# Kernel optimization log

Hardware: AMD Instinct MI355X
Metric: run time of the kernel (lower is better)

The kernel has to match this reference:

```python
import jax, jax.numpy as jnp
import numpy as np

NUM_EXPERTS = 8
TOP_K = 2
P_NORM = 1.0  # moe_normalize_expert_weights
HIDDEN = 1024
FFN_HIDDEN = 2048
BATCH, SEQ = 2, 2048


def setup_inputs() -> dict:
    key = jax.random.key(0)
    ks = jax.random.split(key, 5)
    s = 0.02
    return {
        "x": jax.random.normal(ks[0], (BATCH, SEQ, HIDDEN), dtype=jnp.float32),
        "router_w": jax.random.normal(ks[1], (NUM_EXPERTS, HIDDEN), dtype=jnp.float32) * s,
        "w1": jax.random.normal(ks[2], (NUM_EXPERTS, FFN_HIDDEN, HIDDEN), dtype=jnp.float32) * s,
        "v1": jax.random.normal(ks[3], (NUM_EXPERTS, FFN_HIDDEN, HIDDEN), dtype=jnp.float32) * s,
        "w2": jax.random.normal(ks[4], (NUM_EXPERTS, FFN_HIDDEN, HIDDEN), dtype=jnp.float32) * s,
    }


def reference(x, router_w, w1, v1, w2):
    B, S, H = x.shape
    xf = x.reshape(-1, H)  # [T, H]

    # Router: softmax in fp32, top-k, L-p normalize, cast back.
    logits = xf @ router_w.T  # [T, E]
    probs = jax.nn.softmax(logits.astype(jnp.float32), axis=-1)
    top_w, top_e = jax.lax.top_k(probs, TOP_K)  # [T, K]
    norm = jnp.sum(jnp.abs(top_w) ** P_NORM, axis=-1, keepdims=True) ** (1.0 / P_NORM)
    top_w = (top_w / norm).astype(x.dtype)

    # Per-token combine weight for each expert: c[t,e] = sum_k top_w[t,k]*[top_e[t,k]==e]
    c = jnp.sum(jax.nn.one_hot(top_e, NUM_EXPERTS, dtype=x.dtype) * top_w[..., None], axis=1)  # [T, E]

    # Dense per-expert GLU; routing realized by output gating with c (zero for unrouted tokens).
    out = jnp.zeros_like(xf)
    for e in range(NUM_EXPERTS):
        h = jax.nn.silu(xf @ w1[e].T) * (xf @ v1[e].T)  # [T, F]
        out = out + (h @ w2[e]) * c[:, e:e + 1]  # [T, H]
    return out.reshape(B, S, H)
```

## Files before the change

### kernel.cpp

```cpp
#include <hip/hip_runtime.h>
#include <stdint.h>

#define T_TOKENS 4096
#define HID 1024
#define FFN 2048
#define NE 8

typedef __attribute__((ext_vector_type(8))) short bf16x8;
typedef __attribute__((ext_vector_type(4))) float f32x4;

__device__ __forceinline__ unsigned short f2bf(float f) {
  union { float f; uint32_t u; } v; v.f = f;
  uint32_t r = v.u + 0x7FFFu + ((v.u >> 16) & 1u);
  return (unsigned short)(r >> 16);
}

__device__ __forceinline__ uint32_t pack2(float a, float b) {
  return (uint32_t)f2bf(a) | ((uint32_t)f2bf(b) << 16);
}

__device__ __forceinline__ void gload16(const unsigned short* g, unsigned short* l) {
  __builtin_amdgcn_global_load_lds(
      (const __attribute__((address_space(1))) void*)(g),
      (__attribute__((address_space(3))) void*)(l), 16, 0, 0);
}

__device__ __forceinline__ int frag_off(int r, int g) {
  return r * 32 + ((g ^ ((r >> 1) & 3)) << 3);
}

constexpr size_t XBF_OFF  = 0;
constexpr size_t HBUF_OFF = (size_t)T_TOKENS * HID * 2;
constexpr size_t TOKE_OFF = HBUF_OFF + (size_t)T_TOKENS * 2 * FFN * 2;
constexpr size_t TOKW_OFF = TOKE_OFF + (size_t)T_TOKENS * 2 * 4;
constexpr size_t CNT_OFF  = TOKW_OFF + (size_t)T_TOKENS * 2 * 4;
constexpr size_t OFF_OFF  = CNT_OFF + 64;
constexpr size_t LIST_OFF = OFF_OFF + 64;
constexpr size_t META_END = LIST_OFF + (size_t)NE * T_TOKENS * 4;
constexpr size_t W1BF_OFF = META_END;
constexpr size_t V1BF_OFF = W1BF_OFF + (size_t)NE * FFN * HID * 2;
constexpr size_t W2T_OFF  = V1BF_OFF + (size_t)NE * FFN * HID * 2;
constexpr size_t WS_BIG   = W2T_OFF + (size_t)NE * HID * FFN * 2;
constexpr size_t YBUF_OFF = W1BF_OFF;

__global__ __launch_bounds__(256) void cast_w1v1_kernel(const float* __restrict__ w1,
                                                        const float* __restrict__ v1,
                                                        unsigned short* __restrict__ w1b,
                                                        unsigned short* __restrict__ v1b) {
  constexpr size_t HALF = (size_t)NE * FFN * HID / 8 / 256;
  const float* src = (blockIdx.x < HALF) ? w1 : v1;
  unsigned short* dst = (blockIdx.x < HALF) ? w1b : v1b;
  size_t bi = (blockIdx.x < HALF) ? blockIdx.x : blockIdx.x - HALF;
  size_t i = bi * 256 + threadIdx.x;
  const float4* sv = (const float4*)src;
  float4 a = sv[i * 2], b = sv[i * 2 + 1];
  uint4 o;
  o.x = pack2(a.x, a.y); o.y = pack2(a.z, a.w);
  o.z = pack2(b.x, b.y); o.w = pack2(b.z, b.w);
  ((uint4*)dst)[i] = o;
}

__global__ __launch_bounds__(256) void transpose_cast_w2_kernel(const float* __restrict__ w2,
                                                                unsigned short* __restrict__ w2t) {
  int nb = blockIdx.x;
  int kb = blockIdx.y;
  int e  = blockIdx.z;
  __shared__ unsigned short s[64][68];
  int t = threadIdx.x;
  int tr = t >> 4, tc = (t & 15) * 4;
  const float* src = w2 + ((size_t)e * FFN + kb * 64) * HID + nb * 64;
#pragma unroll
  for (int i = 0; i < 4; ++i) {
    int k = tr + i * 16;
    float4 v = *(const float4*)(src + (size_t)k * HID + tc);
    s[k][tc + 0] = f2bf(v.x); s[k][tc + 1] = f2bf(v.y);
    s[k][tc + 2] = f2bf(v.z); s[k][tc + 3] = f2bf(v.w);
  }
  __syncthreads();
  int n = t >> 2, kc = (t & 3) * 16;
  unsigned short* dst = w2t + ((size_t)e * HID + nb * 64 + n) * FFN + kb * 64 + kc;
  unsigned short tmp[16];
#pragma unroll
  for (int i = 0; i < 16; ++i) tmp[i] = s[kc + i][n];
  uint4 o0, o1;
  o0.x = tmp[0] | (tmp[1] << 16);  o0.y = tmp[2] | (tmp[3] << 16);
  o0.z = tmp[4] | (tmp[5] << 16);  o0.w = tmp[6] | (tmp[7] << 16);
  o1.x = tmp[8] | (tmp[9] << 16);  o1.y = tmp[10] | (tmp[11] << 16);
  o1.z = tmp[12] | (tmp[13] << 16); o1.w = tmp[14] | (tmp[15] << 16);
  *(uint4*)dst = o0;
  *(uint4*)(dst + 8) = o1;
}

__global__ __launch_bounds__(256) void router_kernel(const float* __restrict__ x,
                                                     const float* __restrict__ rw,
                                                     int* __restrict__ tok_e,
                                                     float* __restrict__ tok_w,
                                                     unsigned short* __restrict__ xbf) {
  __shared__ float s_rw[NE * HID];
  int tid = threadIdx.x;
  for (int i = tid; i < NE * HID / 4; i += 256)
    ((float4*)s_rw)[i] = ((const float4*)rw)[i];
  __syncthreads();
  int wave = tid >> 6, lane = tid & 63;
  int t = blockIdx.x * 4 + wave;
  const float* xr = x + (size_t)t * HID;
  unsigned short* xbr = xbf + (size_t)t * HID;
  float acc[NE];
#pragma unroll
  for (int e = 0; e < NE; ++e) acc[e] = 0.0f;
  for (int c = 0; c < HID / 64; ++c) {
    int idx = c * 64 + lane;
    float xv = xr[idx];
    xbr[idx] = f2bf(xv);
#pragma unroll
    for (int e = 0; e < NE; ++e) acc[e] += xv * s_rw[e * HID + idx];
  }
#pragma unroll
  for (int e = 0; e < NE; ++e)
    for (int off = 32; off > 0; off >>= 1) acc[e] += __shfl_down(acc[e], off);
  if (lane == 0) {
    float m = acc[0];
#pragma unroll
    for (int e = 1; e < NE; ++e) m = fmaxf(m, acc[e]);
    float p[NE], Z = 0.0f;
#pragma unroll
    for (int e = 0; e < NE; ++e) { p[e] = expf(acc[e] - m); Z += p[e]; }
    int e0 = 0;
#pragma unroll
    for (int e = 1; e < NE; ++e) if (p[e] > p[e0]) e0 = e;
    int e1 = (e0 == 0) ? 1 : 0;
#pragma unroll
    for (int e = 0; e < NE; ++e) if (e != e0 && p[e] > p[e1]) e1 = e;
    float w0 = p[e0] / Z, w1 = p[e1] / Z;
    float nrm = w0 + w1;
    tok_e[t * 2] = e0; tok_e[t * 2 + 1] = e1;
    tok_w[t * 2] = w0 / nrm; tok_w[t * 2 + 1] = w1 / nrm;
  }
}

__global__ __launch_bounds__(256) void scatter_kernel(const int* __restrict__ tok_e,
                                                      int* __restrict__ counts,
                                                      int* __restrict__ lists) {
  int p = blockIdx.x * 256 + threadIdx.x;
  if (p < T_TOKENS * 2) {
    int e = tok_e[p];
    int pos = atomicAdd(&counts[e], 1);
    lists[e * T_TOKENS + pos] = p;
  }
}

__global__ void offsets_kernel(const int* __restrict__ counts, int* __restrict__ offs) {
  if (threadIdx.x == 0 && blockIdx.x == 0) {
    int r = 0;
    for (int e = 0; e < NE; ++e) { offs[e] = r; r += counts[e]; }
  }
}

__global__ __launch_bounds__(256) void combine_kernel(const float* __restrict__ ybuf,
                                                      float* __restrict__ out) {
  int t = blockIdx.x;
  int c = threadIdx.x;
  const float4* y0 = (const float4*)(ybuf + (size_t)(2 * t) * HID);
  const float4* y1 = (const float4*)(ybuf + (size_t)(2 * t + 1) * HID);
  float4 a = y0[c], b = y1[c];
  float4 r; r.x = a.x + b.x; r.y = a.y + b.y; r.z = a.z + b.z; r.w = a.w + b.w;
  ((float4*)(out + (size_t)t * HID))[c] = r;
}


__global__ __launch_bounds__(512) void gemm1b_kernel(
    const unsigned short* __restrict__ xbf,
    const unsigned short* __restrict__ w1b, const unsigned short* __restrict__ v1b,
    const int* __restrict__ counts, const int* __restrict__ offs,
    const int* __restrict__ lists, unsigned short* __restrict__ hbuf) {
  constexpr int BUFSZ = 128 * 32;
  constexpr int NT = HID / 32;
  int nt = blockIdx.x, mt = blockIdx.y, e = blockIdx.z;
  int ne = counts[e];
  if (mt * 128 >= ne) return;
  __shared__ unsigned short s_a[2 * BUFSZ];
  __shared__ unsigned short s_b1[2 * BUFSZ];
  __shared__ unsigned short s_b2[2 * BUFSZ];
  int tid = threadIdx.x;
  int srow = tid >> 2, slot = tid & 3;
  int lchunk = slot ^ ((srow >> 1) & 3);
  const int* lst = lists + e * T_TOKENS + mt * 128;
  int tok = lst[(mt * 128 + srow < ne) ? srow : 0] >> 1;
  const unsigned short* aptr = xbf + (size_t)tok * HID + lchunk * 8;
  size_t brow = ((size_t)e * FFN + nt * 128 + srow) * HID + lchunk * 8;
  const unsigned short* b1p = w1b + brow;
  const unsigned short* b2p = v1b + brow;

  int lane = tid & 63, wv = tid >> 6;
  int wm = (wv >> 2) * 64, wn = (wv & 3) * 32;
  int rl = lane & 15, g = lane >> 4;
  int aoff[4], boff[2];
#pragma unroll
  for (int m = 0; m < 4; ++m) aoff[m] = frag_off(wm + m * 16 + rl, g);
#pragma unroll
  for (int n = 0; n < 2; ++n) boff[n] = frag_off(wn + n * 16 + rl, g);

  f32x4 zero = {0.0f, 0.0f, 0.0f, 0.0f};
  f32x4 acc1[4][2], acc2[4][2];
#pragma unroll
  for (int i = 0; i < 4; ++i)
#pragma unroll
    for (int j = 0; j < 2; ++j) { acc1[i][j] = zero; acc2[i][j] = zero; }

  auto stage = [&](int s, int t) {
    int off = t * 32;
    gload16(aptr + off, s_a  + s * BUFSZ + tid * 8);
    gload16(b1p  + off, s_b1 + s * BUFSZ + tid * 8);
    gload16(b2p  + off, s_b2 + s * BUFSZ + tid * 8);
  };
  auto compute = [&](int s) {
    const unsigned short* pa  = s_a  + s * BUFSZ;
    const unsigned short* pb1 = s_b1 + s * BUFSZ;
    const unsigned short* pb2 = s_b2 + s * BUFSZ;
    bf16x8 af[4], bfr1[2], bfr2[2];
#pragma unroll
    for (int m = 0; m < 4; ++m) af[m] = *(const bf16x8*)(pa + aoff[m]);
#pragma unroll
    for (int n = 0; n < 2; ++n) {
      bfr1[n] = *(const bf16x8*)(pb1 + boff[n]);
      bfr2[n] = *(const bf16x8*)(pb2 + boff[n]);
    }
#pragma unroll
    for (int m = 0; m < 4; ++m)
#pragma unroll
      for (int n = 0; n < 2; ++n) {
        acc1[m][n] = __builtin_amdgcn_mfma_f32_16x16x32_bf16(af[m], bfr1[n], acc1[m][n], 0, 0, 0);
        acc2[m][n] = __builtin_amdgcn_mfma_f32_16x16x32_bf16(af[m], bfr2[n], acc2[m][n], 0, 0, 0);
      }
  };

  stage(0, 0);
  __syncthreads();
  for (int t = 0; t < NT; t += 2) {
    stage(1, t + 1);
    compute(0);
    __syncthreads();
    if (t + 2 < NT) stage(0, t + 2);
    compute(1);
    __syncthreads();
  }

  int hb = offs[e];
#pragma unroll
  for (int m = 0; m < 4; ++m) {
#pragma unroll
    for (int j = 0; j < 4; ++j) {
      int r = mt * 128 + wm + m * 16 + (lane >> 4) * 4 + j;
      if (r < ne) {
        size_t rowo = (size_t)(hb + r) * FFN;
#pragma unroll
        for (int n = 0; n < 2; ++n) {
          int col = nt * 128 + wn + n * 16 + rl;
          float c1 = acc1[m][n][j], c2 = acc2[m][n][j];
          float h = c1 / (1.0f + __expf(-c1)) * c2;
          hbuf[rowo + col] = f2bf(h);
        }
      }
    }
  }
}

__global__ __launch_bounds__(512) void gemm2b_kernel(
    const unsigned short* __restrict__ hbuf, const unsigned short* __restrict__ w2t,
    const int* __restrict__ counts, const int* __restrict__ offs,
    const int* __restrict__ lists, const float* __restrict__ tok_w,
    float* __restrict__ ybuf) {
  constexpr int BUFSZ = 128 * 32;
  constexpr int NT = FFN / 32;
  int nt = blockIdx.x, mt = blockIdx.y, e = blockIdx.z;
  int ne = counts[e];
  if (mt * 128 >= ne) return;
  __shared__ unsigned short s_a[2 * BUFSZ];
  __shared__ unsigned short s_b[2 * BUFSZ];
  int tid = threadIdx.x;
  int hb = offs[e];
  int srow = tid >> 2, slot = tid & 3;
  int lchunk = slot ^ ((srow >> 1) & 3);
  int ar = mt * 128 + ((mt * 128 + srow < ne) ? srow : 0);
  const unsigned short* aptr = hbuf + (size_t)(hb + ar) * FFN + lchunk * 8;
  const unsigned short* bptr = w2t + ((size_t)e * HID + nt * 128 + srow) * FFN + lchunk * 8;

  int lane = tid & 63, wv = tid >> 6;
  int wm = (wv >> 2) * 64, wn = (wv & 3) * 32;
  int rl = lane & 15, g = lane >> 4;
  int aoff[4], boff[2];
#pragma unroll
  for (int m = 0; m < 4; ++m) aoff[m] = frag_off(wm + m * 16 + rl, g);
#pragma unroll
  for (int n = 0; n < 2; ++n) boff[n] = frag_off(wn + n * 16 + rl, g);

  f32x4 zero = {0.0f, 0.0f, 0.0f, 0.0f};
  f32x4 acc[4][2];
#pragma unroll
  for (int i = 0; i < 4; ++i)
#pragma unroll
    for (int j = 0; j < 2; ++j) acc[i][j] = zero;

  auto stage = [&](int s, int t) {
    int off = t * 32;
    gload16(aptr + off, s_a + s * BUFSZ + tid * 8);
    gload16(bptr + off, s_b + s * BUFSZ + tid * 8);
  };
  auto compute = [&](int s) {
    const unsigned short* pa = s_a + s * BUFSZ;
    const unsigned short* pb = s_b + s * BUFSZ;
    bf16x8 af[4], bfr[2];
#pragma unroll
    for (int m = 0; m < 4; ++m) af[m] = *(const bf16x8*)(pa + aoff[m]);
#pragma unroll
    for (int n = 0; n < 2; ++n) bfr[n] = *(const bf16x8*)(pb + boff[n]);
#pragma unroll
    for (int m = 0; m < 4; ++m)
#pragma unroll
      for (int n = 0; n < 2; ++n)
        acc[m][n] = __builtin_amdgcn_mfma_f32_16x16x32_bf16(af[m], bfr[n], acc[m][n], 0, 0, 0);
  };

  stage(0, 0);
  __syncthreads();
  for (int t = 0; t < NT; t += 2) {
    stage(1, t + 1);
    compute(0);
    __syncthreads();
    if (t + 2 < NT) stage(0, t + 2);
    compute(1);
    __syncthreads();
  }

#pragma unroll
  for (int m = 0; m < 4; ++m) {
#pragma unroll
    for (int j = 0; j < 4; ++j) {
      int r = mt * 128 + wm + m * 16 + (lane >> 4) * 4 + j;
      if (r < ne) {
        int p = lists[e * T_TOKENS + r];
        float w = tok_w[p];
        float* yrow = ybuf + (size_t)p * HID;
#pragma unroll
        for (int n = 0; n < 2; ++n) {
          int col = nt * 128 + wn + n * 16 + rl;
          yrow[col] = acc[m][n][j] * w;
        }
      }
    }
  }
}


__global__ __launch_bounds__(512) void gemm1_kernel(
    const unsigned short* __restrict__ xbf,
    const float* __restrict__ w1, const float* __restrict__ v1,
    const int* __restrict__ counts, const int* __restrict__ offs,
    const int* __restrict__ lists, unsigned short* __restrict__ hbuf) {
  int nt = blockIdx.x, mt = blockIdx.y, e = blockIdx.z;
  int ne = counts[e];
  if (mt * 128 >= ne) return;
  int nrows = ne - mt * 128; if (nrows > 128) nrows = 128;
  __shared__ unsigned short s_a[128 * 40];
  __shared__ unsigned short s_b1[128 * 40];
  __shared__ unsigned short s_b2[128 * 40];
  const int* lst = lists + e * T_TOKENS + mt * 128;
  int tid = threadIdx.x;
  int sr = tid >> 2, sc = tid & 3;
  int pr = lst[(sr < nrows) ? sr : 0];
  const unsigned short* asrc = xbf + (size_t)(pr >> 1) * HID + sc * 8;
  size_t brow = ((size_t)e * FFN + nt * 128 + sr) * HID + sc * 8;
  const float* b1s = w1 + brow;
  const float* b2s = v1 + brow;
  int lane = tid & 63, wv = tid >> 6;
  int wm = (wv >> 2) * 64, wn = (wv & 3) * 32;
  int rl = lane & 15, kg = (lane >> 4) * 8;
  f32x4 zero = {0.0f, 0.0f, 0.0f, 0.0f};
  f32x4 acc1[4][2], acc2[4][2];
#pragma unroll
  for (int i = 0; i < 4; ++i)
#pragma unroll
    for (int j = 0; j < 2; ++j) { acc1[i][j] = zero; acc2[i][j] = zero; }
  int sdst = sr * 40 + sc * 8;
  for (int kk = 0; kk < HID; kk += 32) {
    uint4 av = *(const uint4*)(asrc + kk);
    float4 f0 = *(const float4*)(b1s + kk);
    float4 f1 = *(const float4*)(b1s + kk + 4);
    float4 g0 = *(const float4*)(b2s + kk);
    float4 g1 = *(const float4*)(b2s + kk + 4);
    *(uint4*)(s_a + sdst) = av;
    uint4 bv; bv.x = pack2(f0.x, f0.y); bv.y = pack2(f0.z, f0.w);
    bv.z = pack2(f1.x, f1.y); bv.w = pack2(f1.z, f1.w);
    *(uint4*)(s_b1 + sdst) = bv;
    uint4 cv; cv.x = pack2(g0.x, g0.y); cv.y = pack2(g0.z, g0.w);
    cv.z = pack2(g1.x, g1.y); cv.w = pack2(g1.z, g1.w);
    *(uint4*)(s_b2 + sdst) = cv;
    __syncthreads();
    bf16x8 af[4], bf1[2], bf2[2];
#pragma unroll
    for (int m = 0; m < 4; ++m)
      af[m] = *(const bf16x8*)(s_a + (wm + m * 16 + rl) * 40 + kg);
#pragma unroll
    for (int n = 0; n < 2; ++n) {
      bf1[n] = *(const bf16x8*)(s_b1 + (wn + n * 16 + rl) * 40 + kg);
      bf2[n] = *(const bf16x8*)(s_b2 + (wn + n * 16 + rl) * 40 + kg);
    }
#pragma unroll
    for (int m = 0; m < 4; ++m)
#pragma unroll
      for (int n = 0; n < 2; ++n) {
        acc1[m][n] = __builtin_amdgcn_mfma_f32_16x16x32_bf16(af[m], bf1[n], acc1[m][n], 0, 0, 0);
        acc2[m][n] = __builtin_amdgcn_mfma_f32_16x16x32_bf16(af[m], bf2[n], acc2[m][n], 0, 0, 0);
      }
    __syncthreads();
  }
  int hb = offs[e];
#pragma unroll
  for (int m = 0; m < 4; ++m) {
#pragma unroll
    for (int j = 0; j < 4; ++j) {
      int r = mt * 128 + wm + m * 16 + (lane >> 4) * 4 + j;
      if (r < ne) {
        size_t rowo = (size_t)(hb + r) * FFN;
#pragma unroll
        for (int n = 0; n < 2; ++n) {
          int col = nt * 128 + wn + n * 16 + rl;
          float c1 = acc1[m][n][j], c2 = acc2[m][n][j];
          float h = c1 / (1.0f + __expf(-c1)) * c2;
          hbuf[rowo + col] = f2bf(h);
        }
      }
    }
  }
}

__global__ __launch_bounds__(512) void gemm2_kernel(
    const unsigned short* __restrict__ hbuf, const float* __restrict__ w2,
    const int* __restrict__ counts, const int* __restrict__ offs,
    const int* __restrict__ lists, const float* __restrict__ tok_w,
    float* __restrict__ out) {
  int nt = blockIdx.x, mt = blockIdx.y, e = blockIdx.z;
  int ne = counts[e];
  if (mt * 128 >= ne) return;
  int nrows = ne - mt * 128; if (nrows > 128) nrows = 128;
  __shared__ unsigned short s_a[128 * 40];
  __shared__ unsigned short s_b[128 * 40];
  int tid = threadIdx.x;
  int hb = offs[e];
  int sr = tid >> 2, sc = tid & 3;
  int ar = mt * 128 + ((sr < nrows) ? sr : 0);
  const unsigned short* asrc = hbuf + (size_t)(hb + ar) * FFN + sc * 8;
  int bk = tid >> 4, bn = tid & 15;
  const float* bsrc = w2 + ((size_t)e * FFN + bk) * HID + nt * 128 + bn;
  int lane = tid & 63, wv = tid >> 6;
  int wm = (wv >> 2) * 64, wn = (wv & 3) * 32;
  int rl = lane & 15, kg = (lane >> 4) * 8;
  f32x4 zero = {0.0f, 0.0f, 0.0f, 0.0f};
  f32x4 acc[4][2];
#pragma unroll
  for (int i = 0; i < 4; ++i)
#pragma unroll
    for (int j = 0; j < 2; ++j) acc[i][j] = zero;
  int sdst = sr * 40 + sc * 8;
  for (int kk = 0; kk < FFN; kk += 32) {
    uint4 av = *(const uint4*)(asrc + kk);
    const float* bs = bsrc + (size_t)kk * HID;
    float bvals[8];
#pragma unroll
    for (int i = 0; i < 8; ++i) bvals[i] = bs[i * 16];
    *(uint4*)(s_a + sdst) = av;
#pragma unroll
    for (int i = 0; i < 8; ++i) s_b[(bn + i * 16) * 40 + bk] = f2bf(bvals[i]);
    __syncthreads();
    bf16x8 af[4], bfr[2];
#pragma unroll
    for (int m = 0; m < 4; ++m)
      af[m] = *(const bf16x8*)(s_a + (wm + m * 16 + rl) * 40 + kg);
#pragma unroll
    for (int n = 0; n < 2; ++n)
      bfr[n] = *(const bf16x8*)(s_b + (wn + n * 16 + rl) * 40 + kg);
#pragma unroll
    for (int m = 0; m < 4; ++m)
#pragma unroll
      for (int n = 0; n < 2; ++n)
        acc[m][n] = __builtin_amdgcn_mfma_f32_16x16x32_bf16(af[m], bfr[n], acc[m][n], 0, 0, 0);
    __syncthreads();
  }
#pragma unroll
  for (int m = 0; m < 4; ++m) {
#pragma unroll
    for (int j = 0; j < 4; ++j) {
      int r = mt * 128 + wm + m * 16 + (lane >> 4) * 4 + j;
      if (r < ne) {
        int p = lists[e * T_TOKENS + r];
        float w = tok_w[p];
        float* orow = out + (size_t)(p >> 1) * HID;
#pragma unroll
        for (int n = 0; n < 2; ++n) {
          int col = nt * 128 + wn + n * 16 + rl;
          atomicAdd(orow + col, acc[m][n][j] * w);
        }
      }
    }
  }
}

extern "C" void kernel_launch(void* const* d_in, const int* in_sizes, int n_in,
                              void* d_out, int out_size, void* d_ws, size_t ws_size,
                              hipStream_t stream) {
  const float* x  = (const float*)d_in[0];
  const float* rw = (const float*)d_in[1];
  const float* w1 = (const float*)d_in[2];
  const float* v1 = (const float*)d_in[3];
  const float* w2 = (const float*)d_in[4];
  float* out = (float*)d_out;
  char* ws = (char*)d_ws;
  if (ws_size < META_END) return;

  unsigned short* xbf  = (unsigned short*)(ws + XBF_OFF);
  unsigned short* hbuf = (unsigned short*)(ws + HBUF_OFF);
  int*   tok_e  = (int*)(ws + TOKE_OFF);
  float* tok_w  = (float*)(ws + TOKW_OFF);
  int*   counts = (int*)(ws + CNT_OFF);
  int*   offs   = (int*)(ws + OFF_OFF);
  int*   lists  = (int*)(ws + LIST_OFF);

  hipMemsetAsync(counts, 0, NE * sizeof(int), stream);

  router_kernel<<<T_TOKENS / 4, 256, 0, stream>>>(x, rw, tok_e, tok_w, xbf);
  scatter_kernel<<<(T_TOKENS * 2 + 255) / 256, 256, 0, stream>>>(tok_e, counts, lists);
  offsets_kernel<<<1, 64, 0, stream>>>(counts, offs);

  if (ws_size >= WS_BIG) {
    unsigned short* w1b = (unsigned short*)(ws + W1BF_OFF);
    unsigned short* v1b = (unsigned short*)(ws + V1BF_OFF);
    unsigned short* w2t = (unsigned short*)(ws + W2T_OFF);
    float* ybuf = (float*)(ws + YBUF_OFF);
    int wblocks = NE * FFN * HID / 8 / 256;
    cast_w1v1_kernel<<<2 * wblocks, 256, 0, stream>>>(w1, v1, w1b, v1b);
    transpose_cast_w2_kernel<<<dim3(HID / 64, FFN / 64, NE), 256, 0, stream>>>(w2, w2t);
    gemm1b_kernel<<<dim3(FFN / 128, T_TOKENS / 128, NE), 512, 0, stream>>>(
        xbf, w1b, v1b, counts, offs, lists, hbuf);
    gemm2b_kernel<<<dim3(HID / 128, T_TOKENS / 128, NE), 512, 0, stream>>>(
        hbuf, w2t, counts, offs, lists, tok_w, ybuf);
    combine_kernel<<<T_TOKENS, 256, 0, stream>>>(ybuf, out);
  } else {
    hipMemsetAsync(d_out, 0, (size_t)T_TOKENS * HID * 4, stream);
    gemm1_kernel<<<dim3(FFN / 128, T_TOKENS / 128, NE), 512, 0, stream>>>(
        xbf, w1, v1, counts, offs, lists, hbuf);
    gemm2_kernel<<<dim3(HID / 128, T_TOKENS / 128, NE), 512, 0, stream>>>(
        hbuf, w2, counts, offs, lists, tok_w, out);
  }
}
```

Before: 287.2 us.

## Pre-pack expert weights into MFMA fragment order and load B directly to registers

Weight conversion kernels now write w1/v1/w2 in a packed per-16-column, per-32-k fragment layout so each lane reads its MFMA B operand with one contiguous 16-byte global load. The GEMM kernels drop B from LDS staging and register-double-buffer B instead, cutting LDS traffic and footprint. gemm1b also shrinks to 256 threads with a 64-wide N tile, doubling its grid. The cost is exposed global-load latency on B and more re-reads of weights across M tiles.

```diff
diff --git a/kernel.cpp b/kernel.cpp
--- a/kernel.cpp
+++ b/kernel.cpp
@@ -37,38 +37,51 @@
 constexpr size_t OFF_OFF  = CNT_OFF + 64;
 constexpr size_t LIST_OFF = OFF_OFF + 64;
 constexpr size_t META_END = LIST_OFF + (size_t)NE * T_TOKENS * 4;
-constexpr size_t W1BF_OFF = META_END;
-constexpr size_t V1BF_OFF = W1BF_OFF + (size_t)NE * FFN * HID * 2;
-constexpr size_t W2T_OFF  = V1BF_OFF + (size_t)NE * FFN * HID * 2;
-constexpr size_t WS_BIG   = W2T_OFF + (size_t)NE * HID * FFN * 2;
-constexpr size_t YBUF_OFF = W1BF_OFF;
-
-__global__ __launch_bounds__(256) void cast_w1v1_kernel(const float* __restrict__ w1,
+constexpr size_t PB1_OFF  = META_END;
+constexpr size_t PB2_OFF  = PB1_OFF + (size_t)NE * FFN * HID * 2;
+constexpr size_t PW2_OFF  = PB2_OFF + (size_t)NE * FFN * HID * 2;
+constexpr size_t WS_BIG   = PW2_OFF + (size_t)NE * HID * FFN * 2;
+constexpr size_t YBUF_OFF = PB1_OFF;
+
+__global__ __launch_bounds__(256) void pack_w1v1_kernel(const float* __restrict__ w1,
                                                         const float* __restrict__ v1,
-                                                        unsigned short* __restrict__ w1b,
-                                                        unsigned short* __restrict__ v1b) {
-  constexpr size_t HALF = (size_t)NE * FFN * HID / 8 / 256;
-  const float* src = (blockIdx.x < HALF) ? w1 : v1;
-  unsigned short* dst = (blockIdx.x < HALF) ? w1b : v1b;
-  size_t bi = (blockIdx.x < HALF) ? blockIdx.x : blockIdx.x - HALF;
-  size_t i = bi * 256 + threadIdx.x;
-  const float4* sv = (const float4*)src;
-  float4 a = sv[i * 2], b = sv[i * 2 + 1];
+                                                        unsigned short* __restrict__ pb1,
+                                                        unsigned short* __restrict__ pb2) {
+  int colblk = blockIdx.x;
+  int kslab  = blockIdx.y;
+  int ez     = blockIdx.z;
+  const float* src = (ez < NE) ? w1 : v1;
+  unsigned short* dst = (ez < NE) ? pb1 : pb2;
+  int e = ez & (NE - 1);
+  __shared__ unsigned short lds[2048];
+  int t = threadIdx.x;
+  int c  = colblk * 16 + (t >> 4);
+  int k0 = kslab * 128 + (t & 15) * 8;
+  const float* sp = src + ((size_t)e * FFN + c) * HID + k0;
+  float4 a = *(const float4*)sp;
+  float4 b = *(const float4*)(sp + 4);
   uint4 o;
   o.x = pack2(a.x, a.y); o.y = pack2(a.z, a.w);
   o.z = pack2(b.x, b.y); o.w = pack2(b.z, b.w);
-  ((uint4*)dst)[i] = o;
-}
-
-__global__ __launch_bounds__(256) void transpose_cast_w2_kernel(const float* __restrict__ w2,
-                                                                unsigned short* __restrict__ w2t) {
-  int nb = blockIdx.x;
+  int chunk = ((t & 15) >> 2) * 64 + ((t & 3) * 16 + (t >> 4));
+  int pos = chunk ^ ((chunk >> 4) & 15);
+  *(uint4*)(lds + pos * 8) = o;
+  __syncthreads();
+  int rpos = t ^ ((t >> 4) & 15);
+  uint4 v = *(const uint4*)(lds + rpos * 8);
+  unsigned short* dp = dst + (((size_t)e * (FFN / 16) + colblk) * (HID / 32) + kslab * 4) * 512 + t * 8;
+  *(uint4*)dp = v;
+}
+
+__global__ __launch_bounds__(256) void pack_w2_kernel(const float* __restrict__ w2,
+                                                      unsigned short* __restrict__ pw2) {
+  int cb = blockIdx.x;
   int kb = blockIdx.y;
   int e  = blockIdx.z;
   __shared__ unsigned short s[64][68];
   int t = threadIdx.x;
   int tr = t >> 4, tc = (t & 15) * 4;
-  const float* src = w2 + ((size_t)e * FFN + kb * 64) * HID + nb * 64;
+  const float* src = w2 + ((size_t)e * FFN + kb * 64) * HID + cb * 64;
 #pragma unroll
   for (int i = 0; i < 4; ++i) {
     int k = tr + i * 16;
@@ -77,18 +90,23 @@
     s[k][tc + 2] = f2bf(v.z); s[k][tc + 3] = f2bf(v.w);
   }
   __syncthreads();
-  int n = t >> 2, kc = (t & 3) * 16;
-  unsigned short* dst = w2t + ((size_t)e * HID + nb * 64 + n) * FFN + kb * 64 + kc;
-  unsigned short tmp[16];
-#pragma unroll
-  for (int i = 0; i < 16; ++i) tmp[i] = s[kc + i][n];
-  uint4 o0, o1;
-  o0.x = tmp[0] | (tmp[1] << 16);  o0.y = tmp[2] | (tmp[3] << 16);
-  o0.z = tmp[4] | (tmp[5] << 16);  o0.w = tmp[6] | (tmp[7] << 16);
-  o1.x = tmp[8] | (tmp[9] << 16);  o1.y = tmp[10] | (tmp[11] << 16);
-  o1.z = tmp[12] | (tmp[13] << 16); o1.w = tmp[14] | (tmp[15] << 16);
-  *(uint4*)dst = o0;
-  *(uint4*)(dst + 8) = o1;
+#pragma unroll
+  for (int half = 0; half < 2; ++half) {
+    int cid = t + half * 256;
+    int colblk_l = cid >> 7;
+    int ks_l = (cid >> 6) & 1;
+    int lane = cid & 63;
+    unsigned short tmp[8];
+#pragma unroll
+    for (int j = 0; j < 8; ++j)
+      tmp[j] = s[ks_l * 32 + (lane >> 4) * 8 + j][colblk_l * 16 + (lane & 15)];
+    uint4 o;
+    o.x = tmp[0] | (tmp[1] << 16); o.y = tmp[2] | (tmp[3] << 16);
+    o.z = tmp[4] | (tmp[5] << 16); o.w = tmp[6] | (tmp[7] << 16);
+    unsigned short* dp = pw2 + (((size_t)e * (HID / 16) + cb * 4 + colblk_l) * (FFN / 32)
+                                + kb * 2 + ks_l) * 512 + lane * 8;
+    *(uint4*)dp = o;
+  }
 }
 
 __global__ __launch_bounds__(256) void router_kernel(const float* __restrict__ x,
@@ -167,10 +185,9 @@
   ((float4*)(out + (size_t)t * HID))[c] = r;
 }
 
-
-__global__ __launch_bounds__(512) void gemm1b_kernel(
+__global__ __launch_bounds__(256) void gemm1b_kernel(
     const unsigned short* __restrict__ xbf,
-    const unsigned short* __restrict__ w1b, const unsigned short* __restrict__ v1b,
+    const unsigned short* __restrict__ pb1, const unsigned short* __restrict__ pb2,
     const int* __restrict__ counts, const int* __restrict__ offs,
     const int* __restrict__ lists, unsigned short* __restrict__ hbuf) {
   constexpr int BUFSZ = 128 * 32;
@@ -179,26 +196,27 @@
   int ne = counts[e];
   if (mt * 128 >= ne) return;
   __shared__ unsigned short s_a[2 * BUFSZ];
-  __shared__ unsigned short s_b1[2 * BUFSZ];
-  __shared__ unsigned short s_b2[2 * BUFSZ];
   int tid = threadIdx.x;
-  int srow = tid >> 2, slot = tid & 3;
-  int lchunk = slot ^ ((srow >> 1) & 3);
+  int r0 = tid >> 2, slot = tid & 3;
+  int lchunk = slot ^ ((r0 >> 1) & 3);
   const int* lst = lists + e * T_TOKENS + mt * 128;
-  int tok = lst[(mt * 128 + srow < ne) ? srow : 0] >> 1;
-  const unsigned short* aptr = xbf + (size_t)tok * HID + lchunk * 8;
-  size_t brow = ((size_t)e * FFN + nt * 128 + srow) * HID + lchunk * 8;
-  const unsigned short* b1p = w1b + brow;
-  const unsigned short* b2p = v1b + brow;
+  int tok0 = lst[(mt * 128 + r0 < ne) ? r0 : 0] >> 1;
+  int tok1 = lst[(mt * 128 + r0 + 64 < ne) ? r0 + 64 : 0] >> 1;
+  const unsigned short* aptr0 = xbf + (size_t)tok0 * HID + lchunk * 8;
+  const unsigned short* aptr1 = xbf + (size_t)tok1 * HID + lchunk * 8;
 
   int lane = tid & 63, wv = tid >> 6;
-  int wm = (wv >> 2) * 64, wn = (wv & 3) * 32;
+  int wm = (wv >> 1) * 64, wn = (wv & 1) * 32;
   int rl = lane & 15, g = lane >> 4;
-  int aoff[4], boff[2];
+  int aoff[4];
 #pragma unroll
   for (int m = 0; m < 4; ++m) aoff[m] = frag_off(wm + m * 16 + rl, g);
-#pragma unroll
-  for (int n = 0; n < 2; ++n) boff[n] = frag_off(wn + n * 16 + rl, g);
+
+  size_t cb = (size_t)e * (FFN / 16) + nt * 4 + (wv & 1) * 2;
+  const unsigned short* p1_0 = pb1 + (cb + 0) * (HID / 32) * 512 + lane * 8;
+  const unsigned short* p1_1 = pb1 + (cb + 1) * (HID / 32) * 512 + lane * 8;
+  const unsigned short* p2_0 = pb2 + (cb + 0) * (HID / 32) * 512 + lane * 8;
+  const unsigned short* p2_1 = pb2 + (cb + 1) * (HID / 32) * 512 + lane * 8;
 
   f32x4 zero = {0.0f, 0.0f, 0.0f, 0.0f};
   f32x4 acc1[4][2], acc2[4][2];
@@ -207,41 +225,47 @@
 #pragma unroll
     for (int j = 0; j < 2; ++j) { acc1[i][j] = zero; acc2[i][j] = zero; }
 
-  auto stage = [&](int s, int t) {
-    int off = t * 32;
-    gload16(aptr + off, s_a  + s * BUFSZ + tid * 8);
-    gload16(b1p  + off, s_b1 + s * BUFSZ + tid * 8);
-    gload16(b2p  + off, s_b2 + s * BUFSZ + tid * 8);
-  };
-  auto compute = [&](int s) {
-    const unsigned short* pa  = s_a  + s * BUFSZ;
-    const unsigned short* pb1 = s_b1 + s * BUFSZ;
-    const unsigned short* pb2 = s_b2 + s * BUFSZ;
-    bf16x8 af[4], bfr1[2], bfr2[2];
+  auto stageA = [&](int s, int t) {
+    gload16(aptr0 + t * 32, s_a + s * BUFSZ + tid * 8);
+    gload16(aptr1 + t * 32, s_a + s * BUFSZ + (tid + 256) * 8);
+  };
+  bf16x8 b1X[2], b2X[2], b1Y[2], b2Y[2];
+  auto loadBX = [&](int t) {
+    b1X[0] = *(const bf16x8*)(p1_0 + (size_t)t * 512);
+    b1X[1] = *(const bf16x8*)(p1_1 + (size_t)t * 512);
+    b2X[0] = *(const bf16x8*)(p2_0 + (size_t)t * 512);
+    b2X[1] = *(const bf16x8*)(p2_1 + (size_t)t * 512);
+  };
+  auto loadBY = [&](int t) {
+    b1Y[0] = *(const bf16x8*)(p1_0 + (size_t)t * 512);
+    b1Y[1] = *(const bf16x8*)(p1_1 + (size_t)t * 512);
+    b2Y[0] = *(const bf16x8*)(p2_0 + (size_t)t * 512);
+    b2Y[1] = *(const bf16x8*)(p2_1 + (size_t)t * 512);
+  };
+  auto compute = [&](int s, bf16x8 (&b1)[2], bf16x8 (&b2)[2]) {
+    const unsigned short* pa = s_a + s * BUFSZ;
+    bf16x8 af[4];
 #pragma unroll
     for (int m = 0; m < 4; ++m) af[m] = *(const bf16x8*)(pa + aoff[m]);
 #pragma unroll
-    for (int n = 0; n < 2; ++n) {
-      bfr1[n] = *(const bf16x8*)(pb1 + boff[n]);
-      bfr2[n] = *(const bf16x8*)(pb2 + boff[n]);
-    }
-#pragma unroll
     for (int m = 0; m < 4; ++m)
 #pragma unroll
       for (int n = 0; n < 2; ++n) {
-        acc1[m][n] = __builtin_amdgcn_mfma_f32_16x16x32_bf16(af[m], bfr1[n], acc1[m][n], 0, 0, 0);
-        acc2[m][n] = __builtin_amdgcn_mfma_f32_16x16x32_bf16(af[m], bfr2[n], acc2[m][n], 0, 0, 0);
+        acc1[m][n] = __builtin_amdgcn_mfma_f32_16x16x32_bf16(af[m], b1[n], acc1[m][n], 0, 0, 0);
+        acc2[m][n] = __builtin_amdgcn_mfma_f32_16x16x32_bf16(af[m], b2[n], acc2[m][n], 0, 0, 0);
       }
   };
 
-  stage(0, 0);
+  stageA(0, 0);
+  loadBX(0);
   __syncthreads();
   for (int t = 0; t < NT; t += 2) {
-    stage(1, t + 1);
-    compute(0);
-    __syncthreads();
-    if (t + 2 < NT) stage(0, t + 2);
-    compute(1);
+    stageA(1, t + 1);
+    loadBY(t + 1);
+    compute(0, b1X, b2X);
+    __syncthreads();
+    if (t + 2 < NT) { stageA(0, t + 2); loadBX(t + 2); }
+    compute(1, b1Y, b2Y);
     __syncthreads();
   }
 
@@ -255,7 +279,7 @@
         size_t rowo = (size_t)(hb + r) * FFN;
 #pragma unroll
         for (int n = 0; n < 2; ++n) {
-          int col = nt * 128 + wn + n * 16 + rl;
+          int col = nt * 64 + wn + n * 16 + rl;
           float c1 = acc1[m][n][j], c2 = acc2[m][n][j];
           float h = c1 / (1.0f + __expf(-c1)) * c2;
           hbuf[rowo + col] = f2bf(h);
@@ -266,7 +290,7 @@
 }
 
 __global__ __launch_bounds__(512) void gemm2b_kernel(
-    const unsigned short* __restrict__ hbuf, const unsigned short* __restrict__ w2t,
+    const unsigned short* __restrict__ hbuf, const unsigned short* __restrict__ pw2,
     const int* __restrict__ counts, const int* __restrict__ offs,
     const int* __restrict__ lists, const float* __restrict__ tok_w,
     float* __restrict__ ybuf) {
@@ -276,23 +300,23 @@
   int ne = counts[e];
   if (mt * 128 >= ne) return;
   __shared__ unsigned short s_a[2 * BUFSZ];
-  __shared__ unsigned short s_b[2 * BUFSZ];
   int tid = threadIdx.x;
   int hb = offs[e];
   int srow = tid >> 2, slot = tid & 3;
   int lchunk = slot ^ ((srow >> 1) & 3);
   int ar = mt * 128 + ((mt * 128 + srow < ne) ? srow : 0);
   const unsigned short* aptr = hbuf + (size_t)(hb + ar) * FFN + lchunk * 8;
-  const unsigned short* bptr = w2t + ((size_t)e * HID + nt * 128 + srow) * FFN + lchunk * 8;
 
   int lane = tid & 63, wv = tid >> 6;
   int wm = (wv >> 2) * 64, wn = (wv & 3) * 32;
   int rl = lane & 15, g = lane >> 4;
-  int aoff[4], boff[2];
+  int aoff[4];
 #pragma unroll
   for (int m = 0; m < 4; ++m) aoff[m] = frag_off(wm + m * 16 + rl, g);
-#pragma unroll
-  for (int n = 0; n < 2; ++n) boff[n] = frag_off(wn + n * 16 + rl, g);
+
+  size_t cb = (size_t)e * (HID / 16) + nt * 8 + (wv & 3) * 2;
+  const unsigned short* p_0 = pw2 + (cb + 0) * (FFN / 32) * 512 + lane * 8;
+  const unsigned short* p_1 = pw2 + (cb + 1) * (FFN / 32) * 512 + lane * 8;
 
   f32x4 zero = {0.0f, 0.0f, 0.0f, 0.0f};
   f32x4 acc[4][2];
@@ -301,34 +325,40 @@
 #pragma unroll
     for (int j = 0; j < 2; ++j) acc[i][j] = zero;
 
-  auto stage = [&](int s, int t) {
-    int off = t * 32;
-    gload16(aptr + off, s_a + s * BUFSZ + tid * 8);
-    gload16(bptr + off, s_b + s * BUFSZ + tid * 8);
-  };
-  auto compute = [&](int s) {
+  auto stageA = [&](int s, int t) {
+    gload16(aptr + t * 32, s_a + s * BUFSZ + tid * 8);
+  };
+  bf16x8 bX[2], bY[2];
+  auto loadBX = [&](int t) {
+    bX[0] = *(const bf16x8*)(p_0 + (size_t)t * 512);
+    bX[1] = *(const bf16x8*)(p_1 + (size_t)t * 512);
+  };
+  auto loadBY = [&](int t) {
+    bY[0] = *(const bf16x8*)(p_0 + (size_t)t * 512);
+    bY[1] = *(const bf16x8*)(p_1 + (size_t)t * 512);
+  };
+  auto compute = [&](int s, bf16x8 (&b)[2]) {
     const unsigned short* pa = s_a + s * BUFSZ;
-    const unsigned short* pb = s_b + s * BUFSZ;
-    bf16x8 af[4], bfr[2];
+    bf16x8 af[4];
 #pragma unroll
     for (int m = 0; m < 4; ++m) af[m] = *(const bf16x8*)(pa + aoff[m]);
 #pragma unroll
-    for (int n = 0; n < 2; ++n) bfr[n] = *(const bf16x8*)(pb + boff[n]);
-#pragma unroll
     for (int m = 0; m < 4; ++m)
 #pragma unroll
       for (int n = 0; n < 2; ++n)
-        acc[m][n] = __builtin_amdgcn_mfma_f32_16x16x32_bf16(af[m], bfr[n], acc[m][n], 0, 0, 0);
-  };
-
-  stage(0, 0);
+        acc[m][n] = __builtin_amdgcn_mfma_f32_16x16x32_bf16(af[m], b[n], acc[m][n], 0, 0, 0);
+  };
+
+  stageA(0, 0);
+  loadBX(0);
   __syncthreads();
   for (int t = 0; t < NT; t += 2) {
-    stage(1, t + 1);
-    compute(0);
-    __syncthreads();
-    if (t + 2 < NT) stage(0, t + 2);
-    compute(1);
+    stageA(1, t + 1);
+    loadBY(t + 1);
+    compute(0, bX);
+    __syncthreads();
+    if (t + 2 < NT) { stageA(0, t + 2); loadBX(t + 2); }
+    compute(1, bY);
     __syncthreads();
   }
 
@@ -532,17 +562,16 @@
   offsets_kernel<<<1, 64, 0, stream>>>(counts, offs);
 
   if (ws_size >= WS_BIG) {
-    unsigned short* w1b = (unsigned short*)(ws + W1BF_OFF);
-    unsigned short* v1b = (unsigned short*)(ws + V1BF_OFF);
-    unsigned short* w2t = (unsigned short*)(ws + W2T_OFF);
+    unsigned short* pb1 = (unsigned short*)(ws + PB1_OFF);
+    unsigned short* pb2 = (unsigned short*)(ws + PB2_OFF);
+    unsigned short* pw2 = (unsigned short*)(ws + PW2_OFF);
     float* ybuf = (float*)(ws + YBUF_OFF);
-    int wblocks = NE * FFN * HID / 8 / 256;
-    cast_w1v1_kernel<<<2 * wblocks, 256, 0, stream>>>(w1, v1, w1b, v1b);
-    transpose_cast_w2_kernel<<<dim3(HID / 64, FFN / 64, NE), 256, 0, stream>>>(w2, w2t);
-    gemm1b_kernel<<<dim3(FFN / 128, T_TOKENS / 128, NE), 512, 0, stream>>>(
-        xbf, w1b, v1b, counts, offs, lists, hbuf);
+    pack_w1v1_kernel<<<dim3(FFN / 16, HID / 128, 2 * NE), 256, 0, stream>>>(w1, v1, pb1, pb2);
+    pack_w2_kernel<<<dim3(HID / 64, FFN / 64, NE), 256, 0, stream>>>(w2, pw2);
+    gemm1b_kernel<<<dim3(FFN / 64, T_TOKENS / 128, NE), 256, 0, stream>>>(
+        xbf, pb1, pb2, counts, offs, lists, hbuf);
     gemm2b_kernel<<<dim3(HID / 128, T_TOKENS / 128, NE), 512, 0, stream>>>(
-        hbuf, w2t, counts, offs, lists, tok_w, ybuf);
+        hbuf, pw2, counts, offs, lists, tok_w, ybuf);
     combine_kernel<<<T_TOKENS, 256, 0, stream>>>(ybuf, out);
   } else {
     hipMemsetAsync(d_out, 0, (size_t)T_TOKENS * HID * 4, stream);
```

Measured after the change: 302.8 us. 5.4% more time.
